# Kernel tuning notes

Hardware: AMD Instinct MI355X
Metric: run time of the kernel (lower is better)

## Reference

```python
import jax, jax.numpy as jnp
import numpy as np

NUM_HEADS = 16
EMB = 1024
HEAD_DIM = EMB // NUM_HEADS


def setup_inputs() -> dict:
    key = jax.random.key(0)
    ks = jax.random.split(key, 9)
    N, L = 2, 2048
    return {
        "keys": jax.random.normal(ks[0], (N, L, EMB), dtype=jnp.float32),
        "queries": jax.random.normal(ks[1], (N, L, EMB), dtype=jnp.float32),
        "values": jax.random.normal(ks[2], (N, L, EMB), dtype=jnp.float32),
        "mask": jax.random.randint(ks[3], (N, L), 0, 2, dtype=jnp.int32),
        "Wk": jax.random.normal(ks[4], (HEAD_DIM, HEAD_DIM), dtype=jnp.float32) * 0.05,
        "Wq": jax.random.normal(ks[5], (HEAD_DIM, HEAD_DIM), dtype=jnp.float32) * 0.05,
        "Wv": jax.random.normal(ks[6], (HEAD_DIM, HEAD_DIM), dtype=jnp.float32) * 0.05,
        "Wo": jax.random.normal(ks[7], (EMB, EMB), dtype=jnp.float32) * 0.02,
        "bo": jax.random.normal(ks[8], (EMB,), dtype=jnp.float32) * 0.02,
    }


def reference(keys, queries, values, mask, Wk, Wq, Wv, Wo, bo):
    N, Q, E = queries.shape
    H, D = NUM_HEADS, HEAD_DIM
    # reshape to heads: [N, L, H, D]
    k = keys.reshape(N, -1, H, D) @ Wk.T
    q = queries.reshape(N, -1, H, D) @ Wq.T
    # faithful to source bug: values are the v-projection of the projected queries
    v = q @ Wv.T
    # energy: [N, H, Q, K]
    energy = jnp.einsum("nqhd,nkhd->nhqk", q, k)
    m = mask[:, None, None, :]  # [N,1,1,K]
    energy = jnp.where(m == 0, jnp.float32(-1e20), energy)
    p = jax.nn.softmax(energy / jnp.sqrt(jnp.float32(E)), axis=3)
    attn = jnp.einsum("nhqk,nkhd->nqhd", p, v).reshape(N, Q, E)
    return attn @ Wo.T + bo
```

## Files before the change

kernel.cpp:

```cpp
#include <hip/hip_runtime.h>
#include <cmath>

constexpr int N_ = 2;
constexpr int L_ = 2048;
constexpr int H_ = 16;
constexpr int E_ = 1024;
constexpr int ROWS_ = N_ * L_ * H_;

typedef __attribute__((ext_vector_type(8))) short bf16x8;
typedef __attribute__((ext_vector_type(4))) float f32x4;
typedef unsigned short ushort_t;
#define MFMA16(a, b, c) __builtin_amdgcn_mfma_f32_16x16x32_bf16(a, b, c, 0, 0, 0)

__device__ __forceinline__ unsigned short f2bf(float x) {
    union { float f; unsigned u; } v; v.f = x;
    return (unsigned short)((v.u + 0x7fffu + ((v.u >> 16) & 1u)) >> 16);
}
__device__ __forceinline__ unsigned pack2(float a, float b) {
    return (unsigned)f2bf(a) | ((unsigned)f2bf(b) << 16);
}

__global__ __launch_bounds__(256) void proj_kernel(
    const float* __restrict__ keys, const float* __restrict__ queries,
    const float* __restrict__ Wk, const float* __restrict__ Wq, const float* __restrict__ Wv,
    ushort_t* __restrict__ qo, ushort_t* __restrict__ ko, ushort_t* __restrict__ vto)
{
    constexpr int P = 72;
    __shared__ __align__(16) ushort_t Xq[64 * P];
    __shared__ __align__(16) ushort_t Xk[64 * P];
    __shared__ __align__(16) ushort_t Wqs[64 * P];
    __shared__ __align__(16) ushort_t Wks[64 * P];
    __shared__ __align__(16) ushort_t Wvs[64 * P];
    const int tid = threadIdx.x;
    const int lt = blockIdx.x & 31;
    const int h  = (blockIdx.x >> 5) & 15;
    const int n  = blockIdx.x >> 9;
    const int r0 = tid >> 4, c4 = (tid & 15) * 4;

#pragma unroll
    for (int j = 0; j < 4; ++j) {
        const int r = r0 + 16 * j;
        const size_t xoff = (size_t)(n * L_ + lt * 64 + r) * E_ + h * 64 + c4;
        const float4 xq = *(const float4*)&queries[xoff];
        const float4 xk = *(const float4*)&keys[xoff];
        const float4 wq = *(const float4*)&Wq[r * 64 + c4];
        const float4 wk = *(const float4*)&Wk[r * 64 + c4];
        const float4 wv = *(const float4*)&Wv[r * 64 + c4];
        *(uint2*)&Xq[r * P + c4]  = make_uint2(pack2(xq.x, xq.y), pack2(xq.z, xq.w));
        *(uint2*)&Xk[r * P + c4]  = make_uint2(pack2(xk.x, xk.y), pack2(xk.z, xk.w));
        *(uint2*)&Wqs[r * P + c4] = make_uint2(pack2(wq.x, wq.y), pack2(wq.z, wq.w));
        *(uint2*)&Wks[r * P + c4] = make_uint2(pack2(wk.x, wk.y), pack2(wk.z, wk.w));
        *(uint2*)&Wvs[r * P + c4] = make_uint2(pack2(wv.x, wv.y), pack2(wv.z, wv.w));
    }
    __syncthreads();

    const int wave = tid >> 6, lane = tid & 63;
    const int quad = lane >> 4, l16 = lane & 15;
    const int arow = (wave * 16 + l16) * P;
    const f32x4 zero = (f32x4){0.f, 0.f, 0.f, 0.f};

    bf16x8 a0 = *(const bf16x8*)&Xq[arow + quad * 8];
    bf16x8 a1 = *(const bf16x8*)&Xq[arow + 32 + quad * 8];
    bf16x8 c0 = *(const bf16x8*)&Xk[arow + quad * 8];
    bf16x8 c1 = *(const bf16x8*)&Xk[arow + 32 + quad * 8];
    f32x4 qf[4], kf[4];
#pragma unroll
    for (int nt = 0; nt < 4; ++nt) {
        const int brow = (nt * 16 + l16) * P;
        f32x4 acc = MFMA16(a0, *(const bf16x8*)&Wqs[brow + quad * 8], zero);
        qf[nt] = MFMA16(a1, *(const bf16x8*)&Wqs[brow + 32 + quad * 8], acc);
        acc = MFMA16(c0, *(const bf16x8*)&Wks[brow + quad * 8], zero);
        kf[nt] = MFMA16(c1, *(const bf16x8*)&Wks[brow + 32 + quad * 8], acc);
    }
    __syncthreads();

    const int crow = wave * 16 + quad * 4;
#pragma unroll
    for (int nt = 0; nt < 4; ++nt)
#pragma unroll
        for (int reg = 0; reg < 4; ++reg) {
            Xq[(crow + reg) * P + nt * 16 + l16]  = f2bf(qf[nt][reg]);
            Wqs[(crow + reg) * P + nt * 16 + l16] = f2bf(kf[nt][reg]);
        }
    asm volatile("s_waitcnt lgkmcnt(0)" ::: "memory");

    bf16x8 va0 = *(const bf16x8*)&Xq[arow + quad * 8];
    bf16x8 va1 = *(const bf16x8*)&Xq[arow + 32 + quad * 8];
    f32x4 vf[4];
#pragma unroll
    for (int nt = 0; nt < 4; ++nt) {
        const int brow = (nt * 16 + l16) * P;
        f32x4 acc = MFMA16(va0, *(const bf16x8*)&Wvs[brow + quad * 8], zero);
        vf[nt] = MFMA16(va1, *(const bf16x8*)&Wvs[brow + 32 + quad * 8], acc);
    }
#pragma unroll
    for (int nt = 0; nt < 4; ++nt)
#pragma unroll
        for (int reg = 0; reg < 4; ++reg)
            Xk[(nt * 16 + l16) * P + crow + reg] = f2bf(vf[nt][reg]);
    __syncthreads();

#pragma unroll
    for (int j = 0; j < 4; ++j) {
        const int r = r0 + 16 * j;
        const size_t qkoff = (size_t)(n * L_ + lt * 64 + r) * E_ + h * 64 + c4;
        *(uint2*)&qo[qkoff] = *(const uint2*)&Xq[r * P + c4];
        *(uint2*)&ko[qkoff] = *(const uint2*)&Wqs[r * P + c4];
        const size_t vtoff = ((size_t)(n * H_ + h) * 64 + r) * L_ + lt * 64 + c4;
        *(uint2*)&vto[vtoff] = *(const uint2*)&Xk[r * P + c4];
    }
}

__global__ __launch_bounds__(256) void attn_kernel(
    const ushort_t* __restrict__ q, const ushort_t* __restrict__ k,
    const ushort_t* __restrict__ vt, const float* __restrict__ maskf,
    ushort_t* __restrict__ attn)
{
    constexpr int P = 72;
    constexpr float CEXP = 0.04508422002778010648f;
    __shared__ __align__(16) ushort_t Ks[64 * P];
    __shared__ __align__(16) ushort_t VTs[64 * P];
    __shared__ __align__(16) ushort_t Ps[128 * P];
    __shared__ float Ls[128];

    const int g = blockIdx.x;
    const int xcd = g & 7, j0 = g >> 3;
    const int nh = xcd * 4 + (j0 & 3);
    const int qt = j0 >> 2;
    const int n = nh >> 4, h = nh & 15;

    const int tid = threadIdx.x;
    const int wave = tid >> 6, lane = tid & 63;
    const int l16 = lane & 15, quad = lane >> 4;
    const int r0 = tid >> 4, c4 = (tid & 15) * 4;

    const ushort_t* kh = k  + (size_t)n * L_ * E_ + h * 64;
    const ushort_t* vh = vt + (size_t)(n * H_ + h) * 64 * L_;
    const float*    mh = maskf + n * L_;
    const size_t qrow0 = (size_t)n * L_ + qt * 128 + wave * 32;

    bf16x8 qb[2][2];
#pragma unroll
    for (int s = 0; s < 2; ++s)
#pragma unroll
        for (int c = 0; c < 2; ++c)
            qb[s][c] = *(const bf16x8*)&q[(qrow0 + s * 16 + l16) * E_ + h * 64 + c * 32 + quad * 8];

    uint2 kr[4], vr[4];
#pragma unroll
    for (int j = 0; j < 4; ++j) {
        const int r = r0 + 16 * j;
        kr[j] = *(const uint2*)&kh[(size_t)r * E_ + c4];
        vr[j] = *(const uint2*)&vh[(size_t)r * L_ + c4];
    }
    f32x4 mf[4];
#pragma unroll
    for (int mk = 0; mk < 4; ++mk) mf[mk] = *(const f32x4*)&mh[mk * 16 + quad * 4];

    float lacc[2] = {0.f, 0.f};
    f32x4 O[2][4];
#pragma unroll
    for (int s = 0; s < 2; ++s)
#pragma unroll
        for (int dt = 0; dt < 4; ++dt) O[s][dt] = (f32x4){0.f, 0.f, 0.f, 0.f};

    for (int t = 0; t < 32; ++t) {
#pragma unroll
        for (int j = 0; j < 4; ++j) {
            const int r = r0 + 16 * j;
            *(uint2*)&Ks[r * P + c4]  = kr[j];
            *(uint2*)&VTs[r * P + c4] = vr[j];
        }
        __syncthreads();

        const int tn = (t < 31) ? t + 1 : 31;
#pragma unroll
        for (int j = 0; j < 4; ++j) {
            const int r = r0 + 16 * j;
            kr[j] = *(const uint2*)&kh[(size_t)(tn * 64 + r) * E_ + c4];
            vr[j] = *(const uint2*)&vh[(size_t)r * L_ + tn * 64 + c4];
        }
        f32x4 mfn[4];
#pragma unroll
        for (int mk = 0; mk < 4; ++mk)
            mfn[mk] = *(const f32x4*)&mh[tn * 64 + mk * 16 + quad * 4];

        bf16x8 kA[4][2];
#pragma unroll
        for (int mk = 0; mk < 4; ++mk)
#pragma unroll
            for (int c = 0; c < 2; ++c)
                kA[mk][c] = *(const bf16x8*)&Ks[(mk * 16 + l16) * P + c * 32 + quad * 8];

        f32x4 sA[2][4];
#pragma unroll
        for (int s = 0; s < 2; ++s)
#pragma unroll
            for (int mk = 0; mk < 4; ++mk) {
                f32x4 acc = mf[mk];
                acc = MFMA16(kA[mk][0], qb[s][0], acc);
                sA[s][mk] = MFMA16(kA[mk][1], qb[s][1], acc);
            }

#pragma unroll
        for (int s = 0; s < 2; ++s)
#pragma unroll
            for (int mk = 0; mk < 4; ++mk) {
                const float p0 = __builtin_amdgcn_exp2f(sA[s][mk][0] * CEXP);
                const float p1 = __builtin_amdgcn_exp2f(sA[s][mk][1] * CEXP);
                const float p2 = __builtin_amdgcn_exp2f(sA[s][mk][2] * CEXP);
                const float p3 = __builtin_amdgcn_exp2f(sA[s][mk][3] * CEXP);
                lacc[s] += (p0 + p1) + (p2 + p3);
                *(uint2*)&Ps[(wave * 32 + s * 16 + l16) * P + mk * 16 + quad * 4] =
                    make_uint2(pack2(p0, p1), pack2(p2, p3));
            }
        asm volatile("s_waitcnt lgkmcnt(0)" ::: "memory");

        bf16x8 vB[4][2];
#pragma unroll
        for (int dt = 0; dt < 4; ++dt)
#pragma unroll
            for (int c = 0; c < 2; ++c)
                vB[dt][c] = *(const bf16x8*)&VTs[(dt * 16 + l16) * P + c * 32 + quad * 8];
        bf16x8 pa[2][2];
#pragma unroll
        for (int s = 0; s < 2; ++s)
#pragma unroll
            for (int c = 0; c < 2; ++c)
                pa[s][c] = *(const bf16x8*)&Ps[(wave * 32 + s * 16 + l16) * P + c * 32 + quad * 8];
#pragma unroll
        for (int s = 0; s < 2; ++s)
#pragma unroll
            for (int dt = 0; dt < 4; ++dt) {
                O[s][dt] = MFMA16(pa[s][0], vB[dt][0], O[s][dt]);
                O[s][dt] = MFMA16(pa[s][1], vB[dt][1], O[s][dt]);
            }
#pragma unroll
        for (int mk = 0; mk < 4; ++mk) mf[mk] = mfn[mk];
        __syncthreads();
    }

#pragma unroll
    for (int s = 0; s < 2; ++s) {
        float v = lacc[s];
        v += __shfl_xor(v, 16);
        v += __shfl_xor(v, 32);
        if (quad == 0) Ls[wave * 32 + s * 16 + l16] = 1.f / v;
    }
    asm volatile("s_waitcnt lgkmcnt(0)" ::: "memory");
    f32x4 linv[2];
#pragma unroll
    for (int s = 0; s < 2; ++s) linv[s] = *(const f32x4*)&Ls[wave * 32 + s * 16 + quad * 4];

#pragma unroll
    for (int s = 0; s < 2; ++s)
#pragma unroll
        for (int dt = 0; dt < 4; ++dt)
#pragma unroll
            for (int reg = 0; reg < 4; ++reg) {
                const size_t row = qrow0 + s * 16 + quad * 4 + reg;
                attn[row * E_ + h * 64 + dt * 16 + l16] = f2bf(O[s][dt][reg] * linv[s][reg]);
            }
}

__global__ __launch_bounds__(256) void conv_misc_kernel(
    const float* __restrict__ Wo, const int* __restrict__ mask,
    ushort_t* __restrict__ Wob, float* __restrict__ maskf)
{
    if (blockIdx.x < 1024) {
        const int i = (blockIdx.x * 256 + threadIdx.x) * 4;
        const float4 w = *(const float4*)&Wo[i];
        *(uint2*)&Wob[i] = make_uint2(pack2(w.x, w.y), pack2(w.z, w.w));
    } else {
        const int j = (blockIdx.x - 1024) * 256 + threadIdx.x;
        if (j < N_ * L_) maskf[j] = mask[j] ? 0.f : -1e9f;
    }
}

__global__ __launch_bounds__(256) void outproj_kernel(
    const ushort_t* __restrict__ attn, const ushort_t* __restrict__ Wob,
    const float* __restrict__ bo, float* __restrict__ out)
{
    constexpr int P = 72;
    __shared__ __align__(16) ushort_t As[128 * P];
    __shared__ __align__(16) ushort_t Bs[64 * P];
    const int tid = threadIdx.x;
    const int bc = (blockIdx.x & 15) * 64;
    const int br = (blockIdx.x >> 4) * 128;
    const int r0 = tid >> 4, c4 = (tid & 15) * 4;
    const int wave = tid >> 6, lane = tid & 63;
    const int quad = lane >> 4, l16 = lane & 15;

    uint2 ar[8], brg[4];
#pragma unroll
    for (int j = 0; j < 8; ++j)
        ar[j] = *(const uint2*)&attn[(size_t)(br + r0 + 16 * j) * E_ + c4];
#pragma unroll
    for (int j = 0; j < 4; ++j)
        brg[j] = *(const uint2*)&Wob[(size_t)(bc + r0 + 16 * j) * E_ + c4];

    f32x4 acc[2][4];
#pragma unroll
    for (int s = 0; s < 2; ++s)
#pragma unroll
        for (int nt = 0; nt < 4; ++nt) acc[s][nt] = (f32x4){0.f, 0.f, 0.f, 0.f};

    for (int kt = 0; kt < 16; ++kt) {
#pragma unroll
        for (int j = 0; j < 8; ++j) *(uint2*)&As[(r0 + 16 * j) * P + c4] = ar[j];
#pragma unroll
        for (int j = 0; j < 4; ++j) *(uint2*)&Bs[(r0 + 16 * j) * P + c4] = brg[j];
        __syncthreads();
        const int knext = ((kt < 15) ? (kt + 1) : kt) * 64;
#pragma unroll
        for (int j = 0; j < 8; ++j)
            ar[j] = *(const uint2*)&attn[(size_t)(br + r0 + 16 * j) * E_ + knext + c4];
#pragma unroll
        for (int j = 0; j < 4; ++j)
            brg[j] = *(const uint2*)&Wob[(size_t)(bc + r0 + 16 * j) * E_ + knext + c4];

        bf16x8 aw[2][2], bw[4][2];
#pragma unroll
        for (int s = 0; s < 2; ++s)
#pragma unroll
            for (int c = 0; c < 2; ++c)
                aw[s][c] = *(const bf16x8*)&As[(wave * 32 + s * 16 + l16) * P + c * 32 + quad * 8];
#pragma unroll
        for (int nt = 0; nt < 4; ++nt)
#pragma unroll
            for (int c = 0; c < 2; ++c)
                bw[nt][c] = *(const bf16x8*)&Bs[(nt * 16 + l16) * P + c * 32 + quad * 8];
#pragma unroll
        for (int s = 0; s < 2; ++s)
#pragma unroll
            for (int nt = 0; nt < 4; ++nt) {
                acc[s][nt] = MFMA16(aw[s][0], bw[nt][0], acc[s][nt]);
                acc[s][nt] = MFMA16(aw[s][1], bw[nt][1], acc[s][nt]);
            }
        __syncthreads();
    }
#pragma unroll
    for (int s = 0; s < 2; ++s)
#pragma unroll
        for (int nt = 0; nt < 4; ++nt) {
            const float bias = bo[bc + nt * 16 + l16];
#pragma unroll
            for (int reg = 0; reg < 4; ++reg)
                out[(size_t)(br + wave * 32 + s * 16 + quad * 4 + reg) * E_ + bc + nt * 16 + l16] =
                    acc[s][nt][reg] + bias;
        }
}

extern "C" void kernel_launch(void* const* d_in, const int* in_sizes, int n_in,
                              void* d_out, int out_size, void* d_ws, size_t ws_size,
                              hipStream_t stream)
{
    const float* keys    = (const float*)d_in[0];
    const float* queries = (const float*)d_in[1];
    const int*   mask    = (const int*)d_in[3];
    const float* Wk      = (const float*)d_in[4];
    const float* Wq      = (const float*)d_in[5];
    const float* Wv      = (const float*)d_in[6];
    const float* Wo      = (const float*)d_in[7];
    const float* bo      = (const float*)d_in[8];
    float* out = (float*)d_out;

    ushort_t* qbf  = (ushort_t*)d_ws;
    ushort_t* kbf  = qbf + (size_t)ROWS_ * 64;
    ushort_t* vtbf = kbf + (size_t)ROWS_ * 64;
    ushort_t* abf  = vtbf + (size_t)ROWS_ * 64;
    ushort_t* wob  = abf + (size_t)ROWS_ * 64;
    float*    mskf = (float*)(wob + (size_t)E_ * E_);

    conv_misc_kernel<<<1024 + (N_ * L_ + 255) / 256, 256, 0, stream>>>(Wo, mask, wob, mskf);
    proj_kernel<<<N_ * H_ * (L_ / 64), 256, 0, stream>>>(keys, queries, Wk, Wq, Wv,
                                                         qbf, kbf, vtbf);
    attn_kernel<<<N_ * H_ * (L_ / 128), 256, 0, stream>>>(qbf, kbf, vtbf, mskf, abf);
    outproj_kernel<<<(N_ * L_ / 128) * (E_ / 64), 256, 0, stream>>>(abf, wob, bo, out);
}
```

Before: 199.3 us.

## Double-buffer K/V tiles in LDS and fold softmax scale into K projection

The attention loop now keeps two LDS buffers for K and V^T. The next tile is written into the spare buffer after the PV MFMAs, which removes one __syncthreads per iteration and lets global loads overlap compute. The softmax exponent scale is now applied when K is projected, so the per-element multiply before exp2 disappears. The bf16 packing of probabilities switches to the HIP paired float-to-bf16 conversion intrinsic. The trade-off is double the K/V LDS footprint, which could lower occupancy, and slightly different rounding because K is scaled before conversion to bf16.

```diff
diff --git a/kernel.cpp b/kernel.cpp
--- a/kernel.cpp
+++ b/kernel.cpp
@@ -1,4 +1,5 @@
 #include <hip/hip_runtime.h>
+#include <hip/hip_bf16.h>
 #include <cmath>
 
 constexpr int N_ = 2;
@@ -6,6 +7,7 @@
 constexpr int H_ = 16;
 constexpr int E_ = 1024;
 constexpr int ROWS_ = N_ * L_ * H_;
+constexpr float KSCALE = 0.04508422002778010648f;
 
 typedef __attribute__((ext_vector_type(8))) short bf16x8;
 typedef __attribute__((ext_vector_type(4))) float f32x4;
@@ -17,7 +19,9 @@
     return (unsigned short)((v.u + 0x7fffu + ((v.u >> 16) & 1u)) >> 16);
 }
 __device__ __forceinline__ unsigned pack2(float a, float b) {
-    return (unsigned)f2bf(a) | ((unsigned)f2bf(b) << 16);
+    __hip_bfloat162 t = __float22bfloat162_rn(make_float2(a, b));
+    union { __hip_bfloat162 h; unsigned u; } v; v.h = t;
+    return v.u;
 }
 
 __global__ __launch_bounds__(256) void proj_kernel(
@@ -80,7 +84,7 @@
 #pragma unroll
         for (int reg = 0; reg < 4; ++reg) {
             Xq[(crow + reg) * P + nt * 16 + l16]  = f2bf(qf[nt][reg]);
-            Wqs[(crow + reg) * P + nt * 16 + l16] = f2bf(kf[nt][reg]);
+            Wqs[(crow + reg) * P + nt * 16 + l16] = f2bf(kf[nt][reg] * KSCALE);
         }
     asm volatile("s_waitcnt lgkmcnt(0)" ::: "memory");
 
@@ -117,9 +121,8 @@
     ushort_t* __restrict__ attn)
 {
     constexpr int P = 72;
-    constexpr float CEXP = 0.04508422002778010648f;
-    __shared__ __align__(16) ushort_t Ks[64 * P];
-    __shared__ __align__(16) ushort_t VTs[64 * P];
+    __shared__ __align__(16) ushort_t Ks[2][64 * P];
+    __shared__ __align__(16) ushort_t VTs[2][64 * P];
     __shared__ __align__(16) ushort_t Ps[128 * P];
     __shared__ float Ls[128];
 
@@ -157,6 +160,14 @@
 #pragma unroll
     for (int mk = 0; mk < 4; ++mk) mf[mk] = *(const f32x4*)&mh[mk * 16 + quad * 4];
 
+#pragma unroll
+    for (int j = 0; j < 4; ++j) {
+        const int r = r0 + 16 * j;
+        *(uint2*)&Ks[0][r * P + c4]  = kr[j];
+        *(uint2*)&VTs[0][r * P + c4] = vr[j];
+    }
+    __syncthreads();
+
     float lacc[2] = {0.f, 0.f};
     f32x4 O[2][4];
 #pragma unroll
@@ -165,15 +176,9 @@
         for (int dt = 0; dt < 4; ++dt) O[s][dt] = (f32x4){0.f, 0.f, 0.f, 0.f};
 
     for (int t = 0; t < 32; ++t) {
-#pragma unroll
-        for (int j = 0; j < 4; ++j) {
-            const int r = r0 + 16 * j;
-            *(uint2*)&Ks[r * P + c4]  = kr[j];
-            *(uint2*)&VTs[r * P + c4] = vr[j];
-        }
-        __syncthreads();
-
+        const int cur = t & 1, nxt = cur ^ 1;
         const int tn = (t < 31) ? t + 1 : 31;
+
 #pragma unroll
         for (int j = 0; j < 4; ++j) {
             const int r = r0 + 16 * j;
@@ -190,7 +195,7 @@
         for (int mk = 0; mk < 4; ++mk)
 #pragma unroll
             for (int c = 0; c < 2; ++c)
-                kA[mk][c] = *(const bf16x8*)&Ks[(mk * 16 + l16) * P + c * 32 + quad * 8];
+                kA[mk][c] = *(const bf16x8*)&Ks[cur][(mk * 16 + l16) * P + c * 32 + quad * 8];
 
         f32x4 sA[2][4];
 #pragma unroll
@@ -206,10 +211,10 @@
         for (int s = 0; s < 2; ++s)
 #pragma unroll
             for (int mk = 0; mk < 4; ++mk) {
-                const float p0 = __builtin_amdgcn_exp2f(sA[s][mk][0] * CEXP);
-                const float p1 = __builtin_amdgcn_exp2f(sA[s][mk][1] * CEXP);
-                const float p2 = __builtin_amdgcn_exp2f(sA[s][mk][2] * CEXP);
-                const float p3 = __builtin_amdgcn_exp2f(sA[s][mk][3] * CEXP);
+                const float p0 = __builtin_amdgcn_exp2f(sA[s][mk][0]);
+                const float p1 = __builtin_amdgcn_exp2f(sA[s][mk][1]);
+                const float p2 = __builtin_amdgcn_exp2f(sA[s][mk][2]);
+                const float p3 = __builtin_amdgcn_exp2f(sA[s][mk][3]);
                 lacc[s] += (p0 + p1) + (p2 + p3);
                 *(uint2*)&Ps[(wave * 32 + s * 16 + l16) * P + mk * 16 + quad * 4] =
                     make_uint2(pack2(p0, p1), pack2(p2, p3));
@@ -221,7 +226,7 @@
         for (int dt = 0; dt < 4; ++dt)
 #pragma unroll
             for (int c = 0; c < 2; ++c)
-                vB[dt][c] = *(const bf16x8*)&VTs[(dt * 16 + l16) * P + c * 32 + quad * 8];
+                vB[dt][c] = *(const bf16x8*)&VTs[cur][(dt * 16 + l16) * P + c * 32 + quad * 8];
         bf16x8 pa[2][2];
 #pragma unroll
         for (int s = 0; s < 2; ++s)
@@ -235,6 +240,13 @@
                 O[s][dt] = MFMA16(pa[s][0], vB[dt][0], O[s][dt]);
                 O[s][dt] = MFMA16(pa[s][1], vB[dt][1], O[s][dt]);
             }
+
+#pragma unroll
+        for (int j = 0; j < 4; ++j) {
+            const int r = r0 + 16 * j;
+            *(uint2*)&Ks[nxt][r * P + c4]  = kr[j];
+            *(uint2*)&VTs[nxt][r * P + c4] = vr[j];
+        }
 #pragma unroll
         for (int mk = 0; mk < 4; ++mk) mf[mk] = mfn[mk];
         __syncthreads();
```

Measured after the change: 196.5 us. Within noise of the previous version (-1.4%).
